# Optimization experiments

Hardware: AMD Instinct MI355X
Metric: run time of the kernel (lower is better)

The kernel has to match this reference:

```python
import jax, jax.numpy as jnp
import numpy as np

# ---- config (JambaConfig defaults) ----
D_MODEL = 2048
D_STATE = 128
D_CONV = 4
EXPAND = 2
HEADDIM = 64
D_INNER = EXPAND * D_MODEL           # 4096
NHEADS = D_INNER // HEADDIM          # 64
CONV_DIM = D_INNER + 2 * D_STATE     # 4352
IN_PROJ = 2 * D_INNER + 2 * D_STATE + NHEADS  # 8512
INTER = 5632                         # ((2048*8/3)+255)//256*256
EPS = 1e-6
CHUNK = 128                          # SSD chunk length


def rmsnorm(x, w, eps=EPS):
    var = jnp.mean(jnp.square(x), axis=-1, keepdims=True)
    return x * jax.lax.rsqrt(var + eps) * w


def dw_causal_conv(x, w, b):
    # x: [B,L,C], w: [C,K] depthwise, b: [C]; causal (left pad K-1)
    xt = jnp.transpose(x, (0, 2, 1))                       # [B,C,L]
    xt = jnp.pad(xt, ((0, 0), (0, 0), (D_CONV - 1, 0)))
    y = jax.lax.conv_general_dilated(
        xt, w[:, None, :], window_strides=(1,), padding='VALID',
        feature_group_count=w.shape[0], dimension_numbers=('NCH', 'OIH', 'NCH'))
    y = y + b[None, :, None]
    return jnp.transpose(y, (0, 2, 1))                     # [B,L,C]


def segsum(x):
    # x: [..., T] -> [..., T, T] with out[l,s] = sum_{s<i<=l} x[i], -inf above diag
    T = x.shape[-1]
    xx = jnp.broadcast_to(x[..., None], (*x.shape, T))     # xx[...,i,j] = x[...,i]
    xx = jnp.where(jnp.tril(jnp.ones((T, T), bool), -1), xx, 0.0)
    s = jnp.cumsum(xx, axis=-2)
    return jnp.where(jnp.tril(jnp.ones((T, T), bool), 0), s, -jnp.inf)


def ssd(x, dt, A, Bm, Cm):
    # Mamba2 SSD (chunked selective scan). x:[b,l,h,p] dt:[b,l,h] A:[h] Bm/Cm:[b,l,n]
    b, l, h, p = x.shape
    n = Bm.shape[-1]
    c = l // CHUNK
    xr = x.reshape(b, c, CHUNK, h, p)
    dtr = dt.reshape(b, c, CHUNK, h)
    Br = Bm.reshape(b, c, CHUNK, n)
    Cr = Cm.reshape(b, c, CHUNK, n)
    dA = jnp.transpose(dtr * A, (0, 3, 1, 2))              # [b,h,c,q], all <= 0
    A_cum = jnp.cumsum(dA, axis=-1)                        # [b,h,c,q]
    L = jnp.exp(segsum(dA))                                # [b,h,c,q,q] lower-tri decays
    xdt = xr * dtr[..., None]                              # [b,c,q,h,p]
    # intra-chunk (diagonal blocks)
    Y_diag = jnp.einsum('bcln,bcsn,bhcls,bcshp->bclhp', Cr, Br, L, xdt)
    # chunk-final states
    decay_states = jnp.exp(A_cum[..., -1:] - A_cum)        # [b,h,c,q]
    states = jnp.einsum('bcln,bhcl,bclhp->bchpn', Br, decay_states, xdt)
    # inter-chunk recurrence (parallel via decay matrix over chunks)
    A_last = A_cum[..., -1]                                # [b,h,c]
    decay_chunk = jnp.exp(segsum(jnp.pad(A_last, ((0, 0), (0, 0), (1, 0)))))  # [b,h,c+1,c+1]
    states_cat = jnp.concatenate([jnp.zeros_like(states[:, :1]), states], axis=1)  # [b,c+1,h,p,n]
    new_states = jnp.einsum('bhzc,bchpn->bzhpn', decay_chunk, states_cat)
    prev = new_states[:, :-1]                              # state entering each chunk
    state_decay = jnp.exp(A_cum)                           # [b,h,c,q]
    Y_off = jnp.einsum('bcln,bchpn,bhcl->bclhp', Cr, prev, state_decay)
    return (Y_diag + Y_off).reshape(b, l, h, p)


def setup_inputs() -> dict:
    key = jax.random.key(0)
    ks = jax.random.split(key, 10)
    B, L = 2, 2048
    s = 0.02
    return {
        'hidden_states': jax.random.normal(ks[0], (B, L, D_MODEL), jnp.float32),
        'norm1_w': jnp.ones((D_MODEL,), jnp.float32),
        'in_proj_w': jax.random.normal(ks[1], (D_MODEL, IN_PROJ), jnp.float32) * s,
        'conv_w': jax.random.normal(ks[2], (CONV_DIM, D_CONV), jnp.float32) * 0.1,
        'conv_b': jnp.zeros((CONV_DIM,), jnp.float32),
        'dt_bias': jax.random.uniform(ks[3], (NHEADS,), jnp.float32, -4.0, -1.0),
        'A_log': jnp.log(jnp.arange(1, NHEADS + 1, dtype=jnp.float32)),
        'D_param': jnp.ones((NHEADS,), jnp.float32),
        'mixer_norm_w': jnp.ones((D_INNER,), jnp.float32),
        'out_proj_w': jax.random.normal(ks[4], (D_INNER, D_MODEL), jnp.float32) * s,
        'norm2_w': jnp.ones((D_MODEL,), jnp.float32),
        'gate_w': jax.random.normal(ks[5], (D_MODEL, INTER), jnp.float32) * s,
        'up_w': jax.random.normal(ks[6], (D_MODEL, INTER), jnp.float32) * s,
        'down_w': jax.random.normal(ks[7], (INTER, D_MODEL), jnp.float32) * s,
    }


def reference(hidden_states, norm1_w, in_proj_w, conv_w, conv_b, dt_bias, A_log,
              D_param, mixer_norm_w, out_proj_w, norm2_w, gate_w, up_w, down_w):
    B, L, _ = hidden_states.shape
    # --- norm1 + Mamba2 mixer + residual ---
    res = hidden_states
    h = rmsnorm(hidden_states, norm1_w)
    zxbcdt = h @ in_proj_w                                  # [B,L,8512]
    z = zxbcdt[..., :D_INNER]
    xBC = zxbcdt[..., D_INNER:D_INNER + CONV_DIM]
    dt = jax.nn.softplus(zxbcdt[..., -NHEADS:] + dt_bias)   # [B,L,H]
    xBC = jax.nn.silu(dw_causal_conv(xBC, conv_w, conv_b))
    xs = xBC[..., :D_INNER].reshape(B, L, NHEADS, HEADDIM)
    Bm = xBC[..., D_INNER:D_INNER + D_STATE]
    Cm = xBC[..., D_INNER + D_STATE:]
    A = -jnp.exp(A_log)
    y = ssd(xs, dt, A, Bm, Cm)
    y = y + D_param[None, None, :, None] * xs               # skip D term
    y = y.reshape(B, L, D_INNER)
    y = rmsnorm(y * jax.nn.silu(z), mixer_norm_w)           # gated RMSNorm
    h1 = res + y @ out_proj_w
    # --- norm2 + SwiGLU MLP + residual ---
    h2 = rmsnorm(h1, norm2_w)
    mlp = (jax.nn.silu(h2 @ gate_w) * (h2 @ up_w)) @ down_w
    return h1 + mlp
```

## Files before the change

kernel.cpp:

```cpp
#include <hip/hip_runtime.h>

#define LTOT 2048
#define BATCH 2
#define NTOK 4096
#define DMODEL 2048
#define DSTATE 128
#define NH 64
#define HD 64
#define DINNER 4096
#define CONVD 4352
#define XDTC 4416
#define INP 8512
#define INTER_ 5632
#define CHUNK_ 128
#define NCH 16
#define EPSF 1e-6f

typedef __bf16 bf16x8 __attribute__((ext_vector_type(8)));
typedef float f32x4 __attribute__((ext_vector_type(4)));
typedef unsigned short u16x4 __attribute__((ext_vector_type(4)));
typedef unsigned short u16x8 __attribute__((ext_vector_type(8)));

__device__ __forceinline__ unsigned short f2b(float f){
  unsigned int u = __builtin_bit_cast(unsigned int, f);
  u += 0x7fffu + ((u >> 16) & 1u);
  return (unsigned short)(u >> 16);
}
__device__ __forceinline__ float b2f(unsigned short h){
  return __builtin_bit_cast(float, ((unsigned int)h) << 16);
}
__device__ __forceinline__ f32x4 mfma16(bf16x8 a, bf16x8 b, f32x4 c){
  return __builtin_amdgcn_mfma_f32_16x16x32_bf16(a, b, c, 0, 0, 0);
}
typedef const __attribute__((address_space(1))) void* gas_t;
typedef __attribute__((address_space(3))) void* las_t;
__device__ __forceinline__ void gload16(const void* g, void* l){
  __builtin_amdgcn_global_load_lds((gas_t)g, (las_t)l, 16, 0, 0);
}

__global__ __launch_bounds__(256) void wconv_kernel(const float* __restrict__ W,
                                                    unsigned short* __restrict__ WT,
                                                    int K, int N)
{
  __shared__ unsigned short t[64][72];
  int n0 = blockIdx.x * 64, k0 = blockIdx.y * 64;
  int tid = threadIdx.x;
  int kl = tid >> 4, nl4 = (tid & 15) * 4;
  #pragma unroll
  for (int it = 0; it < 4; it++){
    int kk = kl + it * 16;
    float4 v = make_float4(0.f, 0.f, 0.f, 0.f);
    if (n0 < N) v = *(const float4*)&W[(size_t)(k0 + kk) * N + n0 + nl4];
    t[nl4 + 0][kk] = f2b(v.x);
    t[nl4 + 1][kk] = f2b(v.y);
    t[nl4 + 2][kk] = f2b(v.z);
    t[nl4 + 3][kk] = f2b(v.w);
  }
  __syncthreads();
  int nr = tid >> 3, k8 = (tid & 7) * 8;
  #pragma unroll
  for (int it = 0; it < 2; it++){
    int nn = nr + it * 32;
    *(u16x8*)&WT[(size_t)(n0 + nn) * K + k0 + k8] = *(const u16x8*)&t[nn][k8];
  }
}

__global__ __launch_bounds__(256) void rms_kernel(const float* __restrict__ x,
                                                  const float* __restrict__ w,
                                                  unsigned short* __restrict__ out, int width)
{
  int row = blockIdx.x, tid = threadIdx.x;
  const float* xr = x + (size_t)row * width;
  unsigned short* orow = out + (size_t)row * width;
  int nv = width >> 2;
  float ss = 0.f;
  for (int i = tid; i < nv; i += 256){
    float4 v = ((const float4*)xr)[i];
    ss += v.x*v.x + v.y*v.y + v.z*v.z + v.w*v.w;
  }
  #pragma unroll
  for (int off = 32; off > 0; off >>= 1) ss += __shfl_down(ss, off, 64);
  __shared__ float red[4];
  if ((tid & 63) == 0) red[tid >> 6] = ss;
  __syncthreads();
  float tot = red[0] + red[1] + red[2] + red[3];
  float scale = rsqrtf(tot / (float)width + EPSF);
  for (int i = tid; i < nv; i += 256){
    float4 v = ((const float4*)xr)[i];
    float4 wv = ((const float4*)w)[i];
    u16x4 o = { f2b(v.x * scale * wv.x), f2b(v.y * scale * wv.y),
                f2b(v.z * scale * wv.z), f2b(v.w * scale * wv.w) };
    ((u16x4*)orow)[i] = o;
  }
}

__global__ __launch_bounds__(256) void rms_gated_kernel(const float* __restrict__ y,
                                                        const unsigned short* __restrict__ z,
                                                        const float* __restrict__ w,
                                                        unsigned short* __restrict__ out)
{
  int row = blockIdx.x, tid = threadIdx.x;
  const float* yr = y + (size_t)row * DINNER;
  const unsigned short* zr = z + (size_t)row * DINNER;
  unsigned short* orow = out + (size_t)row * DINNER;
  float g[16];
  float ss = 0.f;
  #pragma unroll
  for (int ii = 0; ii < 4; ii++){
    int i = tid + ii * 256;
    float4 yv = ((const float4*)yr)[i];
    u16x4 zv = ((const u16x4*)zr)[i];
    #pragma unroll
    for (int e = 0; e < 4; e++){
      float zf = b2f(zv[e]);
      float yf = (&yv.x)[e];
      float gg = yf * (zf / (1.f + expf(-zf)));
      g[ii * 4 + e] = gg;
      ss += gg * gg;
    }
  }
  #pragma unroll
  for (int off = 32; off > 0; off >>= 1) ss += __shfl_down(ss, off, 64);
  __shared__ float red[4];
  if ((tid & 63) == 0) red[tid >> 6] = ss;
  __syncthreads();
  float tot = red[0] + red[1] + red[2] + red[3];
  float scale = rsqrtf(tot / (float)DINNER + EPSF);
  #pragma unroll
  for (int ii = 0; ii < 4; ii++){
    int i = tid + ii * 256;
    float4 wv = ((const float4*)w)[i];
    u16x4 o;
    #pragma unroll
    for (int e = 0; e < 4; e++) o[e] = f2b(g[ii * 4 + e] * scale * (&wv.x)[e]);
    ((u16x4*)orow)[i] = o;
  }
}

__global__ __launch_bounds__(512, 1) void gemm3_kernel(const unsigned short* __restrict__ A,
                                                       const unsigned short* __restrict__ BT,
                                                       const float* __restrict__ addsrc,
                                                       float* __restrict__ Cf,
                                                       unsigned short* __restrict__ Cb,
                                                       unsigned short* __restrict__ Cb2, int splitN,
                                                       const unsigned short* __restrict__ gate,
                                                       float* __restrict__ dtraw,
                                                       int M, int N, int K)
{
  extern __shared__ unsigned short lds[];
  int tid = threadIdx.x, lane = tid & 63, w = tid >> 6;
  int wm = w >> 2, wn = w & 3;
  int bid = blockIdx.x + blockIdx.y * gridDim.x;
  int nwg = gridDim.x * gridDim.y;
  int q8 = nwg >> 3, r8 = nwg & 7;
  int xcd = bid & 7, boff = bid >> 3;
  int wgid = (xcd < r8 ? xcd * (q8 + 1) : r8 * (q8 + 1) + (xcd - r8) * q8) + boff;
  int bn = (wgid % gridDim.x) * 256;
  int bm = (wgid / gridDim.x) * 128;

  int srow = lane >> 3;
  int sk   = ((lane & 7) ^ srow) << 3;
  int kswz = (lane & 7) << 3;

  f32x4 acc[4][4] = {};
  int NT = K >> 6;

  #pragma unroll
  for (int pt = 0; pt < 2; ++pt){
    unsigned short* bA = &lds[pt * 24576];
    unsigned short* bB = bA + 8192;
    size_t k0 = (size_t)pt << 6;
    #pragma unroll
    for (int a = 0; a < 2; ++a)
      gload16(&A [(size_t)(bm + a * 64 + w * 8 + srow) * K + k0 + sk], &bA[(a * 8 + w) * 512]);
    #pragma unroll
    for (int b = 0; b < 4; ++b)
      gload16(&BT[(size_t)(bn + b * 64 + w * 8 + srow) * K + k0 + sk], &bB[(b * 8 + w) * 512]);
  }
  asm volatile("s_waitcnt vmcnt(6)" ::: "memory");
  __builtin_amdgcn_s_barrier();
  asm volatile("" ::: "memory");

  for (int t = 0; t < NT; ++t){
    unsigned short* bA = &lds[(t % 3) * 24576];
    unsigned short* bB = bA + 8192;
    int t2 = t + 2;
    unsigned short* nA = &lds[(t2 % 3) * 24576];
    unsigned short* nB = nA + 8192;
    size_t k2 = (size_t)t2 << 6;
    bool pf = t2 < NT;
    bf16x8 bfr[2][4];
    #pragma unroll
    for (int q = 0; q < 2; ++q){
      bf16x8 afr[2][2];
      #pragma unroll
      for (int kk2 = 0; kk2 < 2; ++kk2){
        int kcol = (kk2 * 32 + (lane >> 4) * 8) ^ kswz;
        if (q == 0){
          #pragma unroll
          for (int c = 0; c < 4; ++c)
            bfr[kk2][c] = *(const bf16x8*)&bB[(wn * 64 + c * 16 + (lane & 15)) * 64 + kcol];
        }
        #pragma unroll
        for (int r = 0; r < 2; ++r)
          afr[kk2][r] = *(const bf16x8*)&bA[(wm * 64 + q * 32 + r * 16 + (lane & 15)) * 64 + kcol];
      }
      if (pf){
        if (q == 0){
          gload16(&A [(size_t)(bm +       w * 8 + srow) * K + k2 + sk], &nA[w * 512]);
          gload16(&BT[(size_t)(bn +       w * 8 + srow) * K + k2 + sk], &nB[w * 512]);
          gload16(&BT[(size_t)(bn +  64 + w * 8 + srow) * K + k2 + sk], &nB[(8 + w) * 512]);
        } else {
          gload16(&A [(size_t)(bm +  64 + w * 8 + srow) * K + k2 + sk], &nA[(8 + w) * 512]);
          gload16(&BT[(size_t)(bn + 128 + w * 8 + srow) * K + k2 + sk], &nB[(16 + w) * 512]);
          gload16(&BT[(size_t)(bn + 192 + w * 8 + srow) * K + k2 + sk], &nB[(24 + w) * 512]);
        }
      }
      asm volatile("" ::: "memory");
      __builtin_amdgcn_s_barrier();
      asm volatile("s_waitcnt lgkmcnt(0)" ::: "memory");
      __builtin_amdgcn_s_setprio(1);
      #pragma unroll
      for (int kk2 = 0; kk2 < 2; ++kk2)
        #pragma unroll
        for (int r = 0; r < 2; ++r)
          #pragma unroll
          for (int c = 0; c < 4; ++c)
            acc[q * 2 + r][c] = mfma16(afr[kk2][r], bfr[kk2][c], acc[q * 2 + r][c]);
      __builtin_amdgcn_s_setprio(0);
      if (q == 1){
        if (t + 2 < NT)      asm volatile("s_waitcnt vmcnt(6)" ::: "memory");
        else if (t + 1 < NT) asm volatile("s_waitcnt vmcnt(0)" ::: "memory");
      }
      asm volatile("" ::: "memory");
      __builtin_amdgcn_s_barrier();
      asm volatile("" ::: "memory");
    }
  }

  int r0 = bm + wm * 64 + ((lane >> 4) << 2);
  int c0 = bn + wn * 64 + (lane & 15);
  #pragma unroll
  for (int i = 0; i < 4; ++i){
    #pragma unroll
    for (int j = 0; j < 4; ++j){
      int cc = c0 + j * 16;
      if (cc < N){
        #pragma unroll
        for (int e = 0; e < 4; ++e){
          int rr = r0 + i * 16 + e;
          float v = acc[i][j][e];
          if (Cf){
            size_t idx = (size_t)rr * N + cc;
            if (addsrc) v += addsrc[idx];
            Cf[idx] = v;
          } else if (cc < splitN){
            size_t idx = (size_t)rr * splitN + cc;
            float vv = v;
            if (gate){ float gg = b2f(gate[idx]); vv = gg / (1.f + expf(-gg)) * v; }
            Cb[idx] = f2b(vv);
          } else {
            Cb2[(size_t)rr * (N - splitN) + (cc - splitN)] = f2b(v);
            if (dtraw && cc >= N - NH) dtraw[(size_t)rr * NH + (cc - (N - NH))] = v;
          }
        }
      }
    }
  }
}

__global__ __launch_bounds__(256) void dt_kernel(const float* __restrict__ dtraw,
                                                 const float* __restrict__ dt_bias,
                                                 float* __restrict__ dtb)
{
  int idx = blockIdx.x * 256 + threadIdx.x;
  float raw = dtraw[idx] + dt_bias[idx & 63];
  dtb[idx] = (raw > 20.f) ? raw : log1pf(expf(raw));
}

__global__ __launch_bounds__(64) void acum_kernel(const float* __restrict__ dtb,
                                                  const float* __restrict__ A_log,
                                                  float* __restrict__ acum)
{
  int bid = blockIdx.x;
  int c = bid & 15;
  int hh = (bid >> 4) & 63;
  int b = bid >> 10;
  int lane = threadIdx.x;
  float Av = -expf(A_log[hh]);
  int rowbase = b * LTOT + c * CHUNK_;
  float v0 = dtb[(size_t)(rowbase + 2 * lane) * NH + hh] * Av;
  float v1 = dtb[(size_t)(rowbase + 2 * lane + 1) * NH + hh] * Av;
  float s = v0 + v1;
  #pragma unroll
  for (int d = 1; d < 64; d <<= 1){
    float t = __shfl_up(s, d, 64);
    if (lane >= d) s += t;
  }
  float excl = s - (v0 + v1);
  float* dst = acum + ((size_t)(b * NH + hh)) * LTOT + c * CHUNK_;
  dst[2 * lane]     = excl + v0;
  dst[2 * lane + 1] = excl + v0 + v1;
}

__global__ __launch_bounds__(256) void conv_kernel(const unsigned short* __restrict__ xdt,
                                                   const float* __restrict__ cw,
                                                   const float* __restrict__ cb,
                                                   unsigned short* __restrict__ xbc)
{
  int ch = blockIdx.x * 256 + threadIdx.x;
  int l = blockIdx.y, b = blockIdx.z;
  float acc = cb[ch];
  #pragma unroll
  for (int j = 0; j < 4; j++){
    int ls = l + j - 3;
    if (ls >= 0) acc += b2f(xdt[((size_t)(b * LTOT + ls)) * XDTC + ch]) * cw[ch * 4 + j];
  }
  acc = acc / (1.f + expf(-acc));
  xbc[((size_t)(b * LTOT + l)) * CONVD + ch] = f2b(acc);
}

__global__ __launch_bounds__(256) void ssd_sy_kernel(const unsigned short* __restrict__ xbc,
                                                     const float* __restrict__ dtb,
                                                     const float* __restrict__ acum,
                                                     float* __restrict__ y)
{
  int hh = blockIdx.x;
  int c = blockIdx.y >> 1;
  int half = blockIdx.y & 1;
  int b = blockIdx.z;
  __shared__ unsigned short Cs[64][136];
  __shared__ unsigned short Bs[128][136];
  __shared__ float ac[128];
  int tid = threadIdx.x, lane = tid & 63, w = tid >> 6;
  int l0 = half * 64;
  size_t rowbase = (size_t)b * LTOT + c * CHUNK_;
  if (tid < 128) ac[tid] = acum[((size_t)(b * NH + hh)) * LTOT + c * CHUNK_ + tid];
  #pragma unroll
  for (int p = 0; p < 8; p++){
    int lr = p * 8 + (tid >> 5);
    int n4 = (tid & 31) * 4;
    *(u16x4*)&Cs[lr][n4] =
      *(const u16x4*)&xbc[(rowbase + l0 + lr) * CONVD + DINNER + DSTATE + n4];
  }
  #pragma unroll
  for (int p = 0; p < 16; p++){
    int s = p * 8 + (tid >> 5);
    int n4 = (tid & 31) * 4;
    *(u16x4*)&Bs[s][n4] = *(const u16x4*)&xbc[(rowbase + s) * CONVD + DINNER + n4];
  }
  __syncthreads();
  f32x4 accS[8] = {};
  #pragma unroll
  for (int kk = 0; kk < 4; kk++){
    bf16x8 a = *(const bf16x8*)&Cs[w * 16 + (lane & 15)][kk * 32 + (lane >> 4) * 8];
    #pragma unroll
    for (int fc = 0; fc < 8; fc++){
      bf16x8 bb = *(const bf16x8*)&Bs[fc * 16 + (lane & 15)][kk * 32 + (lane >> 4) * 8];
      accS[fc] = mfma16(a, bb, accS[fc]);
    }
  }
  __syncthreads();
  {
    int lr = w * 16 + ((lane >> 4) << 2);
    #pragma unroll
    for (int fc = 0; fc < 8; fc++){
      int s = fc * 16 + (lane & 15);
      #pragma unroll
      for (int j = 0; j < 4; j++){
        int l = l0 + lr + j;
        float v = (s <= l) ? accS[fc][j] * expf(ac[l] - ac[s]) : 0.f;
        Cs[lr + j][s] = f2b(v);
      }
    }
  }
  #pragma unroll
  for (int p = 0; p < 8; p++){
    int lr = p * 16 + (tid >> 4);
    int p4 = (tid & 15) * 4;
    float dtl = dtb[(rowbase + lr) * NH + hh];
    u16x4 v = *(const u16x4*)&xbc[(rowbase + lr) * CONVD + hh * HD + p4];
    Bs[p4 + 0][lr] = f2b(b2f(v[0]) * dtl);
    Bs[p4 + 1][lr] = f2b(b2f(v[1]) * dtl);
    Bs[p4 + 2][lr] = f2b(b2f(v[2]) * dtl);
    Bs[p4 + 3][lr] = f2b(b2f(v[3]) * dtl);
  }
  __syncthreads();
  f32x4 accY[4] = {};
  #pragma unroll
  for (int kk = 0; kk < 4; kk++){
    bf16x8 a = *(const bf16x8*)&Cs[w * 16 + (lane & 15)][kk * 32 + (lane >> 4) * 8];
    #pragma unroll
    for (int fc = 0; fc < 4; fc++){
      bf16x8 bb = *(const bf16x8*)&Bs[fc * 16 + (lane & 15)][kk * 32 + (lane >> 4) * 8];
      accY[fc] = mfma16(a, bb, accY[fc]);
    }
  }
  {
    int lr = w * 16 + ((lane >> 4) << 2);
    #pragma unroll
    for (int fc = 0; fc < 4; fc++){
      int p = fc * 16 + (lane & 15);
      #pragma unroll
      for (int j = 0; j < 4; j++){
        y[(rowbase + l0 + lr + j) * DINNER + hh * HD + p] = accY[fc][j];
      }
    }
  }
}

__global__ __launch_bounds__(256) void ssd_states_kernel(const unsigned short* __restrict__ xbc,
                                                         const float* __restrict__ dtb,
                                                         const float* __restrict__ acum,
                                                         unsigned short* __restrict__ states)
{
  int hh = blockIdx.x, c = blockIdx.y, b = blockIdx.z;
  __shared__ unsigned short BsT[128][136];
  __shared__ unsigned short XT[64][136];
  __shared__ float ac[128];
  int tid = threadIdx.x, lane = tid & 63, w = tid >> 6;
  size_t rowbase = (size_t)b * LTOT + c * CHUNK_;
  if (tid < 128) ac[tid] = acum[((size_t)(b * NH + hh)) * LTOT + c * CHUNK_ + tid];
  #pragma unroll
  for (int p = 0; p < 16; p++){
    int l = p * 8 + (tid >> 5);
    int n4 = (tid & 31) * 4;
    u16x4 v = *(const u16x4*)&xbc[(rowbase + l) * CONVD + DINNER + n4];
    BsT[n4 + 0][l] = v[0];
    BsT[n4 + 1][l] = v[1];
    BsT[n4 + 2][l] = v[2];
    BsT[n4 + 3][l] = v[3];
  }
  #pragma unroll
  for (int p = 0; p < 8; p++){
    int l = p * 16 + (tid >> 4);
    int p4 = (tid & 15) * 4;
    float dtl = dtb[(rowbase + l) * NH + hh];
    u16x4 v = *(const u16x4*)&xbc[(rowbase + l) * CONVD + hh * HD + p4];
    XT[p4 + 0][l] = f2b(b2f(v[0]) * dtl);
    XT[p4 + 1][l] = f2b(b2f(v[1]) * dtl);
    XT[p4 + 2][l] = f2b(b2f(v[2]) * dtl);
    XT[p4 + 3][l] = f2b(b2f(v[3]) * dtl);
  }
  __syncthreads();
  float aclast = ac[127];
  f32x4 accP[8] = {};
  #pragma unroll
  for (int kk = 0; kk < 4; kk++){
    int kbase = kk * 32 + (lane >> 4) * 8;
    union { u16x4 q[2]; unsigned short u[8]; bf16x8 v; } rw, ot;
    rw.q[0] = *(const u16x4*)&XT[w * 16 + (lane & 15)][kbase];
    rw.q[1] = *(const u16x4*)&XT[w * 16 + (lane & 15)][kbase + 4];
    #pragma unroll
    for (int e = 0; e < 8; e++){
      ot.u[e] = f2b(b2f(rw.u[e]) * expf(aclast - ac[kbase + e]));
    }
    #pragma unroll
    for (int fc = 0; fc < 8; fc++){
      bf16x8 bb = *(const bf16x8*)&BsT[fc * 16 + (lane & 15)][kbase];
      accP[fc] = mfma16(ot.v, bb, accP[fc]);
    }
  }
  size_t sbase = ((size_t)((b * NCH + c) * NH + hh)) * HD * DSTATE;
  int p0 = w * 16 + ((lane >> 4) << 2);
  #pragma unroll
  for (int fc = 0; fc < 8; fc++){
    int n = fc * 16 + (lane & 15);
    #pragma unroll
    for (int j = 0; j < 4; j++){
      states[sbase + (size_t)(p0 + j) * DSTATE + n] = f2b(accP[fc][j]);
    }
  }
}

__global__ __launch_bounds__(256) void scan_kernel(unsigned short* __restrict__ states,
                                                   const float* __restrict__ acum)
{
  int bh = blockIdx.x;
  int b = bh >> 6, hh = bh & 63;
  int t = threadIdx.x;
  float run[32];
  #pragma unroll
  for (int j = 0; j < 32; j++) run[j] = 0.f;
  for (int c = 0; c < NCH; c++){
    float alast = acum[(size_t)bh * LTOT + c * CHUNK_ + 127];
    float dec = expf(alast);
    size_t base = ((size_t)((b * NCH + c) * NH + hh)) * (HD * DSTATE);
    #pragma unroll
    for (int j = 0; j < 32; j++){
      size_t idx = base + (size_t)j * 256 + t;
      float sc = b2f(states[idx]);
      states[idx] = f2b(run[j]);
      run[j] = run[j] * dec + sc;
    }
  }
}

__global__ __launch_bounds__(256) void ssd3_kernel(const unsigned short* __restrict__ xbc,
                                                   const unsigned short* __restrict__ states,
                                                   const float* __restrict__ acum,
                                                   const float* __restrict__ Dp,
                                                   float* __restrict__ y)
{
  int hh = blockIdx.x, c = blockIdx.y, b = blockIdx.z;
  __shared__ unsigned short Cs[128][136];
  __shared__ unsigned short Ps[64][136];
  __shared__ float ac[128];
  int tid = threadIdx.x, lane = tid & 63, w = tid >> 6;
  size_t rowbase = (size_t)b * LTOT + c * CHUNK_;
  if (tid < 128) ac[tid] = acum[((size_t)(b * NH + hh)) * LTOT + c * CHUNK_ + tid];
  #pragma unroll
  for (int p = 0; p < 16; p++){
    int l = p * 8 + (tid >> 5);
    int n4 = (tid & 31) * 4;
    *(u16x4*)&Cs[l][n4] =
      *(const u16x4*)&xbc[(rowbase + l) * CONVD + DINNER + DSTATE + n4];
  }
  size_t sbase = ((size_t)((b * NCH + c) * NH + hh)) * (HD * DSTATE);
  #pragma unroll
  for (int p = 0; p < 8; p++){
    int pp = p * 8 + (tid >> 5);
    int n4 = (tid & 31) * 4;
    *(u16x4*)&Ps[pp][n4] = *(const u16x4*)&states[sbase + (size_t)pp * DSTATE + n4];
  }
  __syncthreads();
  f32x4 acc[2][4] = {};
  #pragma unroll
  for (int kk = 0; kk < 4; kk++){
    bf16x8 a0 = *(const bf16x8*)&Cs[w * 32 + (lane & 15)][kk * 32 + (lane >> 4) * 8];
    bf16x8 a1 = *(const bf16x8*)&Cs[w * 32 + 16 + (lane & 15)][kk * 32 + (lane >> 4) * 8];
    #pragma unroll
    for (int fc = 0; fc < 4; fc++){
      bf16x8 bb = *(const bf16x8*)&Ps[fc * 16 + (lane & 15)][kk * 32 + (lane >> 4) * 8];
      acc[0][fc] = mfma16(a0, bb, acc[0][fc]);
      acc[1][fc] = mfma16(a1, bb, acc[1][fc]);
    }
  }
  float dpar = Dp[hh];
  #pragma unroll
  for (int fr = 0; fr < 2; fr++){
    int lr = w * 32 + fr * 16 + ((lane >> 4) << 2);
    #pragma unroll
    for (int fc = 0; fc < 4; fc++){
      int p = fc * 16 + (lane & 15);
      #pragma unroll
      for (int j = 0; j < 4; j++){
        int l = lr + j;
        size_t yi = (rowbase + l) * DINNER + hh * HD + p;
        float xsv = b2f(xbc[(rowbase + l) * CONVD + hh * HD + p]);
        y[yi] += acc[fr][fc][j] * expf(ac[l]) + dpar * xsv;
      }
    }
  }
}

extern "C" void kernel_launch(void* const* d_in, const int* in_sizes, int n_in,
                              void* d_out, int out_size, void* d_ws, size_t ws_size,
                              hipStream_t stream)
{
  (void)in_sizes; (void)n_in; (void)out_size; (void)ws_size;
  const float* hidden    = (const float*)d_in[0];
  const float* norm1_w   = (const float*)d_in[1];
  const float* in_proj_w = (const float*)d_in[2];
  const float* conv_w    = (const float*)d_in[3];
  const float* conv_b    = (const float*)d_in[4];
  const float* dt_bias   = (const float*)d_in[5];
  const float* A_log     = (const float*)d_in[6];
  const float* D_param   = (const float*)d_in[7];
  const float* mixer_w   = (const float*)d_in[8];
  const float* out_proj_w= (const float*)d_in[9];
  const float* norm2_w   = (const float*)d_in[10];
  const float* gate_w    = (const float*)d_in[11];
  const float* up_w      = (const float*)d_in[12];
  const float* down_w    = (const float*)d_in[13];

  char* ws = (char*)d_ws;
  unsigned short* zbuf    = (unsigned short*)(ws);
  unsigned short* WT_gate = (unsigned short*)(ws);
  unsigned short* xdt     = (unsigned short*)(ws + 33554432ull);
  unsigned short* states  = (unsigned short*)(ws + 33554432ull);
  unsigned short* ygn     = (unsigned short*)(ws + 33554432ull);
  unsigned short* WT_up   = (unsigned short*)(ws + 33554432ull);
  unsigned short* xbc     = (unsigned short*)(ws + 69730304ull);
  unsigned short* WT_out  = (unsigned short*)(ws + 69730304ull);
  unsigned short* h2      = (unsigned short*)(ws + 69730304ull);
  unsigned short* WT_down = (unsigned short*)(ws + 69730304ull);
  float* dtraw            = (float*)(ws + 105381888ull);
  float* dtb              = (float*)(ws + 106430464ull);
  float* acum             = (float*)(ws + 107479040ull);
  float* ybuf             = (float*)(ws + 108527616ull);
  unsigned short* hbuf    = (unsigned short*)(ws + 108527616ull);
  unsigned short* gbuf    = (unsigned short*)(ws + 108527616ull);
  unsigned short* WT_in   = (unsigned short*)(ws + 125304832ull);
  float* h1               = (float*)d_out;
  float* outp             = (float*)d_out;

  const int dynLDS = 147456;
  hipFuncSetAttribute((const void*)gemm3_kernel,
                      hipFuncAttributeMaxDynamicSharedMemorySize, dynLDS);

  wconv_kernel<<<dim3(136, 32), 256, 0, stream>>>(in_proj_w, WT_in, DMODEL, INP);
  rms_kernel<<<NTOK, 256, 0, stream>>>(hidden, norm1_w, hbuf, DMODEL);
  gemm3_kernel<<<dim3(34, 32), 512, dynLDS, stream>>>(hbuf, WT_in, nullptr, nullptr,
                                                      zbuf, xdt, DINNER, nullptr, dtraw,
                                                      NTOK, INP, DMODEL);
  dt_kernel<<<NTOK * NH / 256, 256, 0, stream>>>(dtraw, dt_bias, dtb);
  acum_kernel<<<BATCH * NH * NCH, 64, 0, stream>>>(dtb, A_log, acum);
  conv_kernel<<<dim3(CONVD / 256, LTOT, BATCH), 256, 0, stream>>>(xdt, conv_w, conv_b, xbc);
  ssd_sy_kernel<<<dim3(NH, NCH * 2, BATCH), 256, 0, stream>>>(xbc, dtb, acum, ybuf);
  ssd_states_kernel<<<dim3(NH, NCH, BATCH), 256, 0, stream>>>(xbc, dtb, acum, states);
  scan_kernel<<<BATCH * NH, 256, 0, stream>>>(states, acum);
  ssd3_kernel<<<dim3(NH, NCH, BATCH), 256, 0, stream>>>(xbc, states, acum, D_param, ybuf);
  rms_gated_kernel<<<NTOK, 256, 0, stream>>>(ybuf, zbuf, mixer_w, ygn);
  wconv_kernel<<<dim3(32, 64), 256, 0, stream>>>(out_proj_w, WT_out, DINNER, DMODEL);
  gemm3_kernel<<<dim3(8, 32), 512, dynLDS, stream>>>(ygn, WT_out, hidden, h1,
                                                     nullptr, nullptr, 0, nullptr, nullptr,
                                                     NTOK, DMODEL, DINNER);
  rms_kernel<<<NTOK, 256, 0, stream>>>(h1, norm2_w, h2, DMODEL);
  wconv_kernel<<<dim3(88, 32), 256, 0, stream>>>(gate_w, WT_gate, DMODEL, INTER_);
  gemm3_kernel<<<dim3(22, 32), 512, dynLDS, stream>>>(h2, WT_gate, nullptr, nullptr,
                                                      gbuf, nullptr, INTER_, nullptr, nullptr,
                                                      NTOK, INTER_, DMODEL);
  wconv_kernel<<<dim3(88, 32), 256, 0, stream>>>(up_w, WT_up, DMODEL, INTER_);
  gemm3_kernel<<<dim3(22, 32), 512, dynLDS, stream>>>(h2, WT_up, nullptr, nullptr,
                                                      gbuf, nullptr, INTER_, gbuf, nullptr,
                                                      NTOK, INTER_, DMODEL);
  wconv_kernel<<<dim3(32, 88), 256, 0, stream>>>(down_w, WT_down, INTER_, DMODEL);
  gemm3_kernel<<<dim3(8, 32), 512, dynLDS, stream>>>(gbuf, WT_down, h1, outp,
                                                     nullptr, nullptr, 0, nullptr, nullptr,
                                                     NTOK, DMODEL, INTER_);
}
```

Measured before the change: 1.112 ms.

## Halve GEMM K-tile to 32 and LDS to allow two workgroups per CU

The GEMM mainloop now stages 32-wide K tiles instead of 64-wide ones in a 3-buffer ring, with a new XOR swizzle and one read/compute phase per iteration. Dynamic LDS drops to 72KB and launch bounds request 2 blocks per CU, so two 512-thread workgroups can co-reside and hide each other's latency. The cost is twice as many barriers and iterations per K, shallower prefetch in bytes, and register pressure capped by the occupancy hint, which may cause spills.

```diff
diff --git a/kernel.cpp b/kernel.cpp
--- a/kernel.cpp
+++ b/kernel.cpp
@@ -137,7 +137,7 @@
   }
 }
 
-__global__ __launch_bounds__(512, 1) void gemm3_kernel(const unsigned short* __restrict__ A,
+__global__ __launch_bounds__(512, 2) void gemm3_kernel(const unsigned short* __restrict__ A,
                                                        const unsigned short* __restrict__ BT,
                                                        const float* __restrict__ addsrc,
                                                        float* __restrict__ Cf,
@@ -158,85 +158,56 @@
   int bn = (wgid % gridDim.x) * 256;
   int bm = (wgid / gridDim.x) * 128;
 
-  int srow = lane >> 3;
-  int sk   = ((lane & 7) ^ srow) << 3;
-  int kswz = (lane & 7) << 3;
+  int soct8 = ((lane & 3) ^ ((lane >> 2) & 3)) << 3;
+  int prow_l = (lane >> 2);
+  int ko = (((lane >> 4) ^ (lane & 3)) << 3);
+  int rsel = (lane & 15) * 32 + ko;
 
   f32x4 acc[4][4] = {};
-  int NT = K >> 6;
-
-  #pragma unroll
-  for (int pt = 0; pt < 2; ++pt){
-    unsigned short* bA = &lds[pt * 24576];
-    unsigned short* bB = bA + 8192;
-    size_t k0 = (size_t)pt << 6;
-    #pragma unroll
-    for (int a = 0; a < 2; ++a)
-      gload16(&A [(size_t)(bm + a * 64 + w * 8 + srow) * K + k0 + sk], &bA[(a * 8 + w) * 512]);
-    #pragma unroll
-    for (int b = 0; b < 4; ++b)
-      gload16(&BT[(size_t)(bn + b * 64 + w * 8 + srow) * K + k0 + sk], &bB[(b * 8 + w) * 512]);
-  }
-  asm volatile("s_waitcnt vmcnt(6)" ::: "memory");
+  int NT = K >> 5;
+
+  #define STAGE(kt, bsel)                                                              \
+    {                                                                                  \
+      unsigned short* bb_ = &lds[(bsel) * 12288];                                      \
+      size_t k0_ = (size_t)(kt) << 5;                                                  \
+      gload16(&A [(size_t)(bm +       w * 16 + prow_l) * K + k0_ + soct8], &bb_[w * 512]);            \
+      gload16(&BT[(size_t)(bn +       w * 16 + prow_l) * K + k0_ + soct8], &bb_[4096 + w * 512]);     \
+      gload16(&BT[(size_t)(bn + 128 + w * 16 + prow_l) * K + k0_ + soct8], &bb_[8192 + w * 512]);     \
+    }
+
+  STAGE(0, 0)
+  STAGE(1, 1)
+  asm volatile("s_waitcnt vmcnt(3)" ::: "memory");
   __builtin_amdgcn_s_barrier();
   asm volatile("" ::: "memory");
 
   for (int t = 0; t < NT; ++t){
-    unsigned short* bA = &lds[(t % 3) * 24576];
-    unsigned short* bB = bA + 8192;
-    int t2 = t + 2;
-    unsigned short* nA = &lds[(t2 % 3) * 24576];
-    unsigned short* nB = nA + 8192;
-    size_t k2 = (size_t)t2 << 6;
-    bool pf = t2 < NT;
-    bf16x8 bfr[2][4];
-    #pragma unroll
-    for (int q = 0; q < 2; ++q){
-      bf16x8 afr[2][2];
+    const unsigned short* bufc = &lds[(t % 3) * 12288];
+    bf16x8 afr[4], bfr[4];
+    #pragma unroll
+    for (int i = 0; i < 4; ++i)
+      afr[i] = *(const bf16x8*)&bufc[(wm * 64 + i * 16) * 32 + rsel];
+    #pragma unroll
+    for (int c = 0; c < 4; ++c)
+      bfr[c] = *(const bf16x8*)&bufc[4096 + (wn * 64 + c * 16) * 32 + rsel];
+    if (t + 2 < NT) STAGE(t + 2, (t + 2) % 3)
+    asm volatile("" ::: "memory");
+    __builtin_amdgcn_s_barrier();
+    asm volatile("s_waitcnt lgkmcnt(0)" ::: "memory");
+    __builtin_amdgcn_s_setprio(1);
+    #pragma unroll
+    for (int i = 0; i < 4; ++i)
       #pragma unroll
-      for (int kk2 = 0; kk2 < 2; ++kk2){
-        int kcol = (kk2 * 32 + (lane >> 4) * 8) ^ kswz;
-        if (q == 0){
-          #pragma unroll
-          for (int c = 0; c < 4; ++c)
-            bfr[kk2][c] = *(const bf16x8*)&bB[(wn * 64 + c * 16 + (lane & 15)) * 64 + kcol];
-        }
-        #pragma unroll
-        for (int r = 0; r < 2; ++r)
-          afr[kk2][r] = *(const bf16x8*)&bA[(wm * 64 + q * 32 + r * 16 + (lane & 15)) * 64 + kcol];
-      }
-      if (pf){
-        if (q == 0){
-          gload16(&A [(size_t)(bm +       w * 8 + srow) * K + k2 + sk], &nA[w * 512]);
-          gload16(&BT[(size_t)(bn +       w * 8 + srow) * K + k2 + sk], &nB[w * 512]);
-          gload16(&BT[(size_t)(bn +  64 + w * 8 + srow) * K + k2 + sk], &nB[(8 + w) * 512]);
-        } else {
-          gload16(&A [(size_t)(bm +  64 + w * 8 + srow) * K + k2 + sk], &nA[(8 + w) * 512]);
-          gload16(&BT[(size_t)(bn + 128 + w * 8 + srow) * K + k2 + sk], &nB[(16 + w) * 512]);
-          gload16(&BT[(size_t)(bn + 192 + w * 8 + srow) * K + k2 + sk], &nB[(24 + w) * 512]);
-        }
-      }
-      asm volatile("" ::: "memory");
-      __builtin_amdgcn_s_barrier();
-      asm volatile("s_waitcnt lgkmcnt(0)" ::: "memory");
-      __builtin_amdgcn_s_setprio(1);
-      #pragma unroll
-      for (int kk2 = 0; kk2 < 2; ++kk2)
-        #pragma unroll
-        for (int r = 0; r < 2; ++r)
-          #pragma unroll
-          for (int c = 0; c < 4; ++c)
-            acc[q * 2 + r][c] = mfma16(afr[kk2][r], bfr[kk2][c], acc[q * 2 + r][c]);
-      __builtin_amdgcn_s_setprio(0);
-      if (q == 1){
-        if (t + 2 < NT)      asm volatile("s_waitcnt vmcnt(6)" ::: "memory");
-        else if (t + 1 < NT) asm volatile("s_waitcnt vmcnt(0)" ::: "memory");
-      }
-      asm volatile("" ::: "memory");
-      __builtin_amdgcn_s_barrier();
-      asm volatile("" ::: "memory");
-    }
-  }
+      for (int c = 0; c < 4; ++c)
+        acc[i][c] = mfma16(afr[i], bfr[c], acc[i][c]);
+    __builtin_amdgcn_s_setprio(0);
+    if (t + 2 < NT)      asm volatile("s_waitcnt vmcnt(3)" ::: "memory");
+    else if (t + 1 < NT) asm volatile("s_waitcnt vmcnt(0)" ::: "memory");
+    asm volatile("" ::: "memory");
+    __builtin_amdgcn_s_barrier();
+    asm volatile("" ::: "memory");
+  }
+  #undef STAGE
 
   int r0 = bm + wm * 64 + ((lane >> 4) << 2);
   int c0 = bn + wn * 64 + (lane & 15);
@@ -595,7 +566,7 @@
   float* h1               = (float*)d_out;
   float* outp             = (float*)d_out;
 
-  const int dynLDS = 147456;
+  const int dynLDS = 73728;
   hipFuncSetAttribute((const void*)gemm3_kernel,
                       hipFuncAttributeMaxDynamicSharedMemorySize, dynLDS);
 
```

After: 1.088 ms. 2.2% less time.
